# Kernel optimization log

Measured on AMD Instinct MI355X. Metric: run time of the kernel, lower is better.

## Reference

```python
import jax, jax.numpy as jnp
import numpy as np

B, S = 64, 512
DC, DB = 200, 200            # embed_char_dim, embed_bichar_dim
HID = 300                    # linear out / lstm input
H = 300                      # rnn_hidden_dim
VC, VB = 10000, 200000       # char / bichar vocab
INPUT_DIM = (DC + DB) * 2    # 800


def lstm_scan(x_seq, W_hh):
    # x_seq: [S, B, 4H] = x @ W_ih.T + b_ih + b_hh, precomputed for all steps
    Bq = x_seq.shape[1]
    h0 = jnp.zeros((Bq, H), x_seq.dtype)
    c0 = jnp.zeros((Bq, H), x_seq.dtype)

    def step(carry, x_t):
        h, c = carry
        gates = x_t + h @ W_hh.T                 # [B, 4H]
        i, f, g, o = jnp.split(gates, 4, axis=-1)
        i = jax.nn.sigmoid(i)
        f = jax.nn.sigmoid(f)
        g = jnp.tanh(g)
        o = jax.nn.sigmoid(o)
        c = f * c + i * g
        h = o * jnp.tanh(c)
        return (h, c), h

    _, hs = jax.lax.scan(step, (h0, c0), x_seq)
    return hs                                    # [S, B, H]


def setup_inputs() -> dict:
    key = jax.random.key(0)
    ks = jax.random.split(key, 20)
    inp = {
        'char_features': jax.random.randint(ks[0], (B, S), 0, VC),
        'bichar_left_features': jax.random.randint(ks[1], (B, S), 0, VB),
        'bichar_right_features': jax.random.randint(ks[2], (B, S), 0, VB),
        'static_char_features': jax.random.randint(ks[3], (B, S), 0, VC),
        'static_bichar_left_features': jax.random.randint(ks[4], (B, S), 0, VB),
        'static_bichar_right_features': jax.random.randint(ks[5], (B, S), 0, VB),
        # embedding tables (padding-id row zeroing omitted; random rows)
        'char_embed': jax.random.normal(ks[6], (VC, DC), jnp.float32) * 0.1,
        'bichar_embed': jax.random.normal(ks[7], (VB, DB), jnp.float32) * 0.1,
        'static_char_embed': jax.random.uniform(ks[8], (VC, DC), jnp.float32, -0.12, 0.12),
        'static_bichar_embed': jax.random.uniform(ks[9], (VB, DB), jnp.float32, -0.12, 0.12),
        # linear: [HID, INPUT_DIM]
        'W_lin': jax.random.normal(ks[10], (HID, INPUT_DIM), jnp.float32) * (1.0 / np.sqrt(INPUT_DIM)),
        'b_lin': jax.random.normal(ks[11], (HID,), jnp.float32) * 0.01,
        # LSTM cells (b = b_ih + b_hh folded)
        'Wih_l': jax.random.normal(ks[12], (4 * H, HID), jnp.float32) * (1.0 / np.sqrt(HID)),
        'Whh_l': jax.random.normal(ks[13], (4 * H, H), jnp.float32) * (1.0 / np.sqrt(H)),
        'b_l': jax.random.normal(ks[14], (4 * H,), jnp.float32) * 0.01,
        'Wih_r': jax.random.normal(ks[15], (4 * H, HID), jnp.float32) * (1.0 / np.sqrt(HID)),
        'Whh_r': jax.random.normal(ks[16], (4 * H, H), jnp.float32) * (1.0 / np.sqrt(H)),
        'b_r': jax.random.normal(ks[17], (4 * H,), jnp.float32) * 0.01,
    }
    return inp


def reference(char_features, bichar_left_features, bichar_right_features,
              static_char_features, static_bichar_left_features, static_bichar_right_features,
              char_embed, bichar_embed, static_char_embed, static_bichar_embed,
              W_lin, b_lin, Wih_l, Whh_l, b_l, Wih_r, Whh_r, b_r):
    # embedding lookups (dropout is identity in eval mode)
    cf = char_embed[char_features]                       # [B,S,DC]
    scf = static_char_embed[static_char_features]        # [B,S,DC]
    bl = bichar_embed[bichar_left_features]              # [B,S,DB]
    br = bichar_embed[bichar_right_features]             # [B,S,DB]
    sbl = static_bichar_embed[static_bichar_left_features]
    sbr = static_bichar_embed[static_bichar_right_features]

    left = jnp.concatenate([cf, scf, bl, sbl], axis=-1)   # [B,S,INPUT_DIM]
    right = jnp.concatenate([cf, scf, br, sbr], axis=-1)
    left = jnp.tanh(left @ W_lin.T + b_lin)               # [B,S,HID]
    right = jnp.tanh(right @ W_lin.T + b_lin)

    # precompute input contributions for all timesteps, then scan the recurrence
    xl = jnp.einsum('bsd,gd->sbg', left, Wih_l) + b_l     # [S,B,4H]
    hs_l = lstm_scan(xl, Whh_l)                            # [S,B,H]

    xr = jnp.einsum('bsd,gd->sbg', right, Wih_r) + b_r
    hs_r = lstm_scan(xr[::-1], Whh_r)[::-1]               # right-to-left LSTM

    out = jnp.concatenate([hs_l.transpose(1, 0, 2), hs_r.transpose(1, 0, 2)], axis=-1)
    return out                                             # [B,S,2H]
```

## Files before the change

### kernel.cpp

```cpp
#include <hip/hip_runtime.h>
#include <hip/hip_bf16.h>

#define S_LEN 512
#define BATCH 64
#define DC    200
#define HID   300
#define H4    1200
#define IN_DIM 800
#define G_SPLIT 10

typedef __attribute__((ext_vector_type(8))) short short8b;
typedef __attribute__((ext_vector_type(4))) float f32x4;
typedef __attribute__((ext_vector_type(4))) int   i32x4;

__device__ __forceinline__ float sigmoidf_(float x) { return 1.0f / (1.0f + __expf(-x)); }
__device__ __forceinline__ float tanhf_(float x)    { return 2.0f / (1.0f + __expf(-2.0f * x)) - 1.0f; }

__global__ void k_prep_w(const float* __restrict__ Whh_l, const float* __restrict__ Whh_r,
                         const float* __restrict__ Wih_l, const float* __restrict__ Wih_r,
                         __hip_bfloat16* __restrict__ Whh_p, __hip_bfloat16* __restrict__ Wih_p) {
    int i = blockIdx.x * 256 + threadIdx.x;
    if (i >= 2 * 1280 * 320) return;
    int slot = i % 320;
    int R = (i / 320) % 1280;
    int d = i / (320 * 1280);
    int g = R >> 7, local = R & 127;
    float vh = 0.f, vi = 0.f;
    if (local < 120) {
        int q = local / 30, jj = local % 30;
        int n = q * 300 + g * 30 + jj;
        const float* Whh = d ? Whh_r : Whh_l;
        const float* Wih = d ? Wih_r : Wih_l;
        int g2 = slot >> 5, jj2 = slot & 31;
        if (jj2 < 30) vh = Whh[n * 300 + g2 * 30 + jj2];
        if (slot < 300) vi = Wih[n * 300 + slot];
    }
    Whh_p[i] = __float2bfloat16(vh);
    Wih_p[i] = __float2bfloat16(vi);
}

__global__ void k_prep_misc(const float* __restrict__ b_l, const float* __restrict__ b_r,
                            int* __restrict__ hb_st,
                            float* __restrict__ bias_p) {
    int i = blockIdx.x * 256 + threadIdx.x;
    if (i < 102400) hb_st[i] = 0;
    if (i < 2 * 1280) {
        int d = i / 1280, R = i % 1280;
        int g = R >> 7, local = R & 127;
        float v = 0.f;
        if (local < 120) { int q = local / 30, jj = local % 30; v = (d ? b_r : b_l)[q * 300 + g * 30 + jj]; }
        bias_p[i] = v;
    }
}

__global__ __launch_bounds__(256) void k_lin(
    const int* __restrict__ cf, const int* __restrict__ bl, const int* __restrict__ br,
    const int* __restrict__ scf, const int* __restrict__ sbl, const int* __restrict__ sbr,
    const float* __restrict__ ce, const float* __restrict__ be,
    const float* __restrict__ sce, const float* __restrict__ sbe,
    const float* __restrict__ W, const float* __restrict__ bias,
    __hip_bfloat16* __restrict__ outL, __hip_bfloat16* __restrict__ outR)
{
    const int z = blockIdx.y;
    const int* dynIdx  = z ? br  : bl;
    const int* statIdx = z ? sbr : sbl;
    __hip_bfloat16* outp = z ? outR : outL;
    const int m0 = blockIdx.x * 64;

    __shared__ __align__(16) __hip_bfloat16 sA[64][40];
    __shared__ __align__(16) __hip_bfloat16 sB[320][40];
    const int t = threadIdx.x, lane = t & 63, wv = t >> 6;

    const int rA = t >> 2, c8A = (t & 3) * 8;
    const int mA = m0 + rA;
    const int idc = cf[mA], idsc = scf[mA], idd = dynIdx[mA], ids = statIdx[mA];

    f32x4 acc[4][5] = {};

    for (int k0 = 0; k0 < IN_DIM; k0 += 32) {
        {
            int k = k0 + c8A;
            int seg = k / 200, kin = k - seg * 200;
            const float* tab = (seg == 0) ? ce : (seg == 1) ? sce : (seg == 2) ? be : sbe;
            int id = (seg == 0) ? idc : (seg == 1) ? idsc : (seg == 2) ? idd : ids;
            const float* tp = tab + (size_t)id * DC + kin;
            f32x4 v0 = *reinterpret_cast<const f32x4*>(tp);
            f32x4 v1 = *reinterpret_cast<const f32x4*>(tp + 4);
            union { short8b v; __hip_bfloat16 h[8]; } u;
#pragma unroll
            for (int q = 0; q < 4; ++q) { u.h[q] = __float2bfloat16(v0[q]); u.h[4 + q] = __float2bfloat16(v1[q]); }
            *reinterpret_cast<short8b*>(&sA[rA][c8A]) = u.v;
        }
#pragma unroll
        for (int j = 0; j < 5; ++j) {
            int i = t + j * 256;
            int n = i >> 2, ch = (i & 3) * 8;
            f32x4 v0 = {0, 0, 0, 0}, v1 = {0, 0, 0, 0};
            if (n < HID) {
                const float* wp = W + (size_t)n * IN_DIM + k0 + ch;
                v0 = *reinterpret_cast<const f32x4*>(wp);
                v1 = *reinterpret_cast<const f32x4*>(wp + 4);
            }
            union { short8b v; __hip_bfloat16 h[8]; } u;
#pragma unroll
            for (int q = 0; q < 4; ++q) { u.h[q] = __float2bfloat16(v0[q]); u.h[4 + q] = __float2bfloat16(v1[q]); }
            *reinterpret_cast<short8b*>(&sB[n][ch]) = u.v;
        }
        __syncthreads();
        const int kl = (lane >> 4) * 8, bb = lane & 15;
#pragma unroll
        for (int mt = 0; mt < 4; ++mt) {
            short8b af = *reinterpret_cast<const short8b*>(&sA[mt * 16 + bb][kl]);
#pragma unroll
            for (int nt = 0; nt < 5; ++nt) {
                short8b bf = *reinterpret_cast<const short8b*>(&sB[(wv * 5 + nt) * 16 + bb][kl]);
                acc[mt][nt] = __builtin_amdgcn_mfma_f32_16x16x32_bf16(af, bf, acc[mt][nt], 0, 0, 0);
            }
        }
        __syncthreads();
    }
    const int bb = lane & 15;
#pragma unroll
    for (int mt = 0; mt < 4; ++mt)
#pragma unroll
        for (int nt = 0; nt < 5; ++nt) {
            int p = (wv * 5 + nt) * 16 + bb;
            float bv = (p < HID) ? bias[p] : 0.f;
#pragma unroll
            for (int r = 0; r < 4; ++r) {
                int m = m0 + mt * 16 + (lane >> 4) * 4 + r;
                float val = (p < HID) ? tanhf_(acc[mt][nt][r] + bv) : 0.f;
                outp[(size_t)m * 320 + p] = __float2bfloat16(val);
            }
        }
}

__global__ __launch_bounds__(256) void k_xgemm(
    const __hip_bfloat16* __restrict__ A,
    const __hip_bfloat16* __restrict__ Wih_p,
    const float* __restrict__ bias_p,
    __hip_bfloat16* __restrict__ Xout)
{
    const int dir = blockIdx.z;
    const int m0 = blockIdx.x * 64;
    const int n0 = blockIdx.y * 128;
    const __hip_bfloat16* Ad = A + (size_t)dir * 32768 * 320;
    const __hip_bfloat16* Wd = Wih_p + (size_t)dir * 1280 * 320;
    const float* bd = bias_p + dir * 1280;
    __hip_bfloat16* Xd = Xout + (size_t)dir * 512 * 64 * 1280;

    __shared__ __align__(16) __hip_bfloat16 sA[64][40];
    __shared__ __align__(16) __hip_bfloat16 sB[128][40];
    const int t = threadIdx.x, lane = t & 63, wv = t >> 6;
    f32x4 acc[4][2] = {};

    for (int k0 = 0; k0 < 320; k0 += 32) {
        {
            int r = t >> 2, kg = (t & 3) * 8;
            *reinterpret_cast<short8b*>(&sA[r][kg]) =
                *reinterpret_cast<const short8b*>(Ad + (size_t)(m0 + r) * 320 + k0 + kg);
        }
#pragma unroll
        for (int i = 0; i < 2; ++i) {
            int c = t + i * 256;
            int r = c >> 2, kg = (c & 3) * 8;
            *reinterpret_cast<short8b*>(&sB[r][kg]) =
                *reinterpret_cast<const short8b*>(Wd + (size_t)(n0 + r) * 320 + k0 + kg);
        }
        __syncthreads();
        const int kl = (lane >> 4) * 8;
#pragma unroll
        for (int mt = 0; mt < 4; ++mt) {
            short8b af = *reinterpret_cast<const short8b*>(&sA[mt * 16 + (lane & 15)][kl]);
#pragma unroll
            for (int nt = 0; nt < 2; ++nt) {
                short8b bf = *reinterpret_cast<const short8b*>(&sB[(wv * 2 + nt) * 16 + (lane & 15)][kl]);
                acc[mt][nt] = __builtin_amdgcn_mfma_f32_16x16x32_bf16(af, bf, acc[mt][nt], 0, 0, 0);
            }
        }
        __syncthreads();
    }
#pragma unroll
    for (int mt = 0; mt < 4; ++mt)
#pragma unroll
        for (int nt = 0; nt < 2; ++nt) {
            int p = n0 + (wv * 2 + nt) * 16 + (lane & 15);
            float bv = bd[p];
#pragma unroll
            for (int r = 0; r < 4; ++r) {
                int m = m0 + mt * 16 + (lane >> 4) * 4 + r;
                int b = m >> 9, s = m & 511;
                Xd[(size_t)(s * 64 + b) * 1280 + p] = __float2bfloat16(acc[mt][nt][r] + bv);
            }
        }
}

__global__ __launch_bounds__(256) void k_rec(
    const __hip_bfloat16* __restrict__ X,
    const __hip_bfloat16* __restrict__ Whh_p,
    i32x4* __restrict__ hb_st,
    float* __restrict__ out)
{
    const int bid = blockIdx.x;
    const int dir = bid / (4 * G_SPLIT);
    const int grp = (bid / G_SPLIT) % 4;
    const int g   = bid % G_SPLIT;
    const int t = threadIdx.x;
    const int lane = t & 63, wv = t >> 6;
    const int b0 = grp * 16;

    __shared__ __align__(16) __hip_bfloat16 sHi[16][328];
    __shared__ __align__(16) __hip_bfloat16 sLo[16][328];
    __shared__ float sG[16][132];
    unsigned* sHiW = (unsigned*)sHi;
    unsigned* sLoW = (unsigned*)sLo;

    const int n0 = wv * 32;
    const int bb = lane & 15;
    const int hi4 = lane >> 4;

    short8b wB0[10], wB1[10];
    {
        const __hip_bfloat16* Wsrc = Whh_p + ((size_t)dir * 1280 + g * 128) * 320;
#pragma unroll
        for (int kt = 0; kt < 10; ++kt) {
            wB0[kt] = *reinterpret_cast<const short8b*>(Wsrc + (size_t)(n0 + bb) * 320 + kt * 32 + hi4 * 8);
            wB1[kt] = *reinterpret_cast<const short8b*>(Wsrc + (size_t)(n0 + 16 + bb) * 320 + kt * 32 + hi4 * 8);
        }
    }
    for (int i = t; i < 16 * 164; i += 256) { sHiW[i] = 0; sLoW[i] = 0; }
    __syncthreads();

    float cst[6] = {};

    __hip_bfloat16 xa[8];
    {
        const int s0 = dir ? (S_LEN - 1) : 0;
        const __hip_bfloat16* xp = X + (((size_t)dir * 512 + s0) * 64 + b0) * 1280 + g * 128;
#pragma unroll
        for (int r = 0; r < 4; ++r) {
            int m = hi4 * 4 + r;
            xa[r]     = xp[(size_t)m * 1280 + n0 + bb];
            xa[4 + r] = xp[(size_t)m * 1280 + n0 + 16 + bb];
        }
    }

    for (int tau = 0; tau < S_LEN; ++tau) {
        const int s = dir ? (S_LEN - 1 - tau) : tau;
        const int par = tau & 1;

        i32x4 ch[7];
        const i32x4* hbase = hb_st + ((size_t)(dir * 2 + par) * 64 + b0) * 100;
        for (;;) {
            bool ok = true;
#pragma unroll
            for (int k = 0; k < 7; ++k) {
                int idx = t + k * 256;
                if (idx < 1600)
                    asm volatile("global_load_dwordx4 %0, %1, off sc0 sc1"
                                 : "=v"(ch[k]) : "v"(hbase + idx) : "memory");
            }
            asm volatile("s_waitcnt vmcnt(0)" ::: "memory");
#pragma unroll
            for (int k = 0; k < 7; ++k) {
                int idx = t + k * 256;
                if (idx < 1600 && ch[k][0] != tau) ok = false;
            }
            if (ok) break;
            __builtin_amdgcn_s_sleep(1);
        }
        __builtin_amdgcn_sched_barrier(0);

#pragma unroll
        for (int k = 0; k < 7; ++k) {
            int idx = t + k * 256;
            if (idx < 1600) {
                int b = idx / 100, rem = idx - b * 100;
                int g2 = rem / 10, c = rem - g2 * 10;
                int chi = (c < 5) ? c : c - 5;
                unsigned* dst = ((c < 5) ? sHiW : sLoW) + b * 164 + g2 * 16 + chi * 3;
                dst[0] = (unsigned)ch[k][1];
                dst[1] = (unsigned)ch[k][2];
                dst[2] = (unsigned)ch[k][3];
            }
        }
        __syncthreads();

        f32x4 acc0, acc1;
#pragma unroll
        for (int r = 0; r < 4; ++r) {
            acc0[r] = __bfloat162float(xa[r]);
            acc1[r] = __bfloat162float(xa[4 + r]);
        }
#pragma unroll
        for (int kt = 0; kt < 10; ++kt) {
            short8b ahi = *reinterpret_cast<const short8b*>(&sHi[bb][kt * 32 + hi4 * 8]);
            short8b alo = *reinterpret_cast<const short8b*>(&sLo[bb][kt * 32 + hi4 * 8]);
            acc0 = __builtin_amdgcn_mfma_f32_16x16x32_bf16(ahi, wB0[kt], acc0, 0, 0, 0);
            acc1 = __builtin_amdgcn_mfma_f32_16x16x32_bf16(ahi, wB1[kt], acc1, 0, 0, 0);
            acc0 = __builtin_amdgcn_mfma_f32_16x16x32_bf16(alo, wB0[kt], acc0, 0, 0, 0);
            acc1 = __builtin_amdgcn_mfma_f32_16x16x32_bf16(alo, wB1[kt], acc1, 0, 0, 0);
        }
#pragma unroll
        for (int r = 0; r < 4; ++r) {
            int m = hi4 * 4 + r;
            sG[m][n0 + bb] = acc0[r];
            sG[m][n0 + 16 + bb] = acc1[r];
        }
        __syncthreads();

        if (t < 80) {
            int b = t / 5, c5 = t - (b * 5), jj0 = c5 * 6;
            float hv[6];
            unsigned hius[6], lous[6];
#pragma unroll
            for (int u = 0; u < 6; ++u) {
                int jj = jj0 + u;
                float ig = sigmoidf_(sG[b][jj]);
                float fg = sigmoidf_(sG[b][30 + jj]);
                float gg = tanhf_(sG[b][60 + jj]);
                float og = sigmoidf_(sG[b][90 + jj]);
                float cn = fg * cst[u] + ig * gg;
                cst[u] = cn;
                float h = og * tanhf_(cn);
                hv[u] = h;
                __hip_bfloat16 hb_ = __float2bfloat16(h);
                float lof = h - __bfloat162float(hb_);
                __hip_bfloat16 lb_ = __float2bfloat16(lof);
                union { __hip_bfloat16 x; unsigned short u16; } ch1{hb_}, ch2{lb_};
                hius[u] = ch1.u16;
                lous[u] = ch2.u16;
            }
            i32x4 dhi, dlo;
            dhi[0] = tau + 1; dhi[1] = (int)(hius[0] | (hius[1] << 16));
            dhi[2] = (int)(hius[2] | (hius[3] << 16)); dhi[3] = (int)(hius[4] | (hius[5] << 16));
            dlo[0] = tau + 1; dlo[1] = (int)(lous[0] | (lous[1] << 16));
            dlo[2] = (int)(lous[2] | (lous[3] << 16)); dlo[3] = (int)(lous[4] | (lous[5] << 16));
            i32x4* pb = hb_st + ((size_t)(dir * 2 + (par ^ 1)) * 64 + b0 + b) * 100 + g * 10 + c5;
            asm volatile("s_waitcnt vmcnt(0)" ::: "memory");
            asm volatile("global_store_dwordx4 %0, %1, off sc0 sc1" :: "v"(pb), "v"(dhi) : "memory");
            asm volatile("global_store_dwordx4 %0, %1, off sc0 sc1" :: "v"(pb + 5), "v"(dlo) : "memory");
            float* op = out + ((size_t)(b0 + b) * S_LEN + s) * 600 + dir * 300 + g * 30 + jj0;
#pragma unroll
            for (int u = 0; u < 6; ++u) op[u] = hv[u];
        }

        if (tau < S_LEN - 1) {
            const int sn = dir ? (s - 1) : (s + 1);
            const __hip_bfloat16* xp = X + (((size_t)dir * 512 + sn) * 64 + b0) * 1280 + g * 128;
#pragma unroll
            for (int r = 0; r < 4; ++r) {
                int m = hi4 * 4 + r;
                xa[r]     = xp[(size_t)m * 1280 + n0 + bb];
                xa[4 + r] = xp[(size_t)m * 1280 + n0 + 16 + bb];
            }
        }
    }
}

extern "C" void kernel_launch(void* const* d_in, const int* in_sizes, int n_in,
                              void* d_out, int out_size, void* d_ws, size_t ws_size,
                              hipStream_t stream) {
    const int*   cf    = (const int*)d_in[0];
    const int*   bl    = (const int*)d_in[1];
    const int*   br    = (const int*)d_in[2];
    const int*   scf   = (const int*)d_in[3];
    const int*   sbl   = (const int*)d_in[4];
    const int*   sbr   = (const int*)d_in[5];
    const float* ce    = (const float*)d_in[6];
    const float* be    = (const float*)d_in[7];
    const float* sce   = (const float*)d_in[8];
    const float* sbe   = (const float*)d_in[9];
    const float* Wlin  = (const float*)d_in[10];
    const float* blin  = (const float*)d_in[11];
    const float* Wih_l = (const float*)d_in[12];
    const float* Whh_l = (const float*)d_in[13];
    const float* b_l   = (const float*)d_in[14];
    const float* Wih_r = (const float*)d_in[15];
    const float* Whh_r = (const float*)d_in[16];
    const float* b_r   = (const float*)d_in[17];
    float* out = (float*)d_out;

    char* ws = (char*)d_ws;
    __hip_bfloat16* A_b    = (__hip_bfloat16*)(ws);
    __hip_bfloat16* A_l    = A_b;
    __hip_bfloat16* A_r    = A_b + (size_t)32768 * 320;
    __hip_bfloat16* X      = (__hip_bfloat16*)(ws + 41943040);
    __hip_bfloat16* Whh_p  = (__hip_bfloat16*)(ws + 209715200);
    __hip_bfloat16* Wih_p  = (__hip_bfloat16*)(ws + 211353600);
    float*          bias_p = (float*)(ws + 212992000);
    i32x4*          hb_st  = (i32x4*)(ws + 213002240);

    k_prep_w<<<dim3((2 * 1280 * 320 + 255) / 256), dim3(256), 0, stream>>>(
        Whh_l, Whh_r, Wih_l, Wih_r, Whh_p, Wih_p);
    k_prep_misc<<<dim3(1280), dim3(256), 0, stream>>>(b_l, b_r, (int*)hb_st, bias_p);
    k_lin<<<dim3(512, 2), dim3(256), 0, stream>>>(cf, bl, br, scf, sbl, sbr,
                                                  ce, be, sce, sbe, Wlin, blin,
                                                  A_l, A_r);
    k_xgemm<<<dim3(512, 10, 2), dim3(256), 0, stream>>>(A_b, Wih_p, bias_p, X);
    k_rec<<<dim3(80), dim3(256), 0, stream>>>(X, Whh_p, hb_st, out);
}
```

Baseline: 2.288 ms.

## Poll only unfinished hidden-state chunks and write own slice directly to LDS

The recurrent kernel's spin-wait now remembers which 16-byte hidden-state chunks already carry the current step tag and reloads only the missing ones. Chunks produced by the same block are no longer read back from global memory; the producing threads write them straight into shared memory. The global layout interleaves the hi and lo chunks in pairs. The sleep between polls grows, which cuts coherent-load traffic during the cross-block barrier but may add wake-up latency on the critical path.

```diff
diff --git a/kernel.cpp b/kernel.cpp
--- a/kernel.cpp
+++ b/kernel.cpp
@@ -40,10 +40,10 @@
 }
 
 __global__ void k_prep_misc(const float* __restrict__ b_l, const float* __restrict__ b_r,
-                            int* __restrict__ hb_st,
+                            int* __restrict__ hb,
                             float* __restrict__ bias_p) {
     int i = blockIdx.x * 256 + threadIdx.x;
-    if (i < 102400) hb_st[i] = 0;
+    if (i < 102400) hb[i] = 0;
     if (i < 2 * 1280) {
         int d = i / 1280, R = i % 1280;
         int g = R >> 7, local = R & 127;
@@ -198,7 +198,7 @@
 __global__ __launch_bounds__(256) void k_rec(
     const __hip_bfloat16* __restrict__ X,
     const __hip_bfloat16* __restrict__ Whh_p,
-    i32x4* __restrict__ hb_st,
+    i32x4* __restrict__ hb,
     float* __restrict__ out)
 {
     const int bid = blockIdx.x;
@@ -231,6 +231,16 @@
     for (int i = t; i < 16 * 164; i += 256) { sHiW[i] = 0; sLoW[i] = 0; }
     __syncthreads();
 
+    unsigned own_mask = 0;
+#pragma unroll
+    for (int k = 0; k < 7; ++k) {
+        int idx = t + k * 256;
+        if (idx < 1600) {
+            int pair = (idx % 100) >> 1;
+            if (pair / 5 == g) own_mask |= 1u << k;
+        }
+    }
+
     float cst[6] = {};
 
     __hip_bfloat16 xa[8];
@@ -249,39 +259,43 @@
         const int s = dir ? (S_LEN - 1 - tau) : tau;
         const int par = tau & 1;
 
-        i32x4 ch[7];
-        const i32x4* hbase = hb_st + ((size_t)(dir * 2 + par) * 64 + b0) * 100;
+        i32x4 q[7];
+        unsigned done = own_mask;
+        const i32x4* hbase = hb + ((size_t)(dir * 2 + par) * 64 + b0) * 100;
         for (;;) {
-            bool ok = true;
 #pragma unroll
             for (int k = 0; k < 7; ++k) {
                 int idx = t + k * 256;
-                if (idx < 1600)
+                if (idx < 1600 && !((done >> k) & 1))
                     asm volatile("global_load_dwordx4 %0, %1, off sc0 sc1"
-                                 : "=v"(ch[k]) : "v"(hbase + idx) : "memory");
+                                 : "=v"(q[k]) : "v"(hbase + idx) : "memory");
             }
             asm volatile("s_waitcnt vmcnt(0)" ::: "memory");
+            bool all = true;
 #pragma unroll
             for (int k = 0; k < 7; ++k) {
                 int idx = t + k * 256;
-                if (idx < 1600 && ch[k][0] != tau) ok = false;
-            }
-            if (ok) break;
-            __builtin_amdgcn_s_sleep(1);
+                if (idx < 1600 && !((done >> k) & 1)) {
+                    if (q[k][0] == tau) done |= 1u << k;
+                    else all = false;
+                }
+            }
+            if (all) break;
+            __builtin_amdgcn_s_sleep(4);
         }
         __builtin_amdgcn_sched_barrier(0);
 
 #pragma unroll
         for (int k = 0; k < 7; ++k) {
             int idx = t + k * 256;
-            if (idx < 1600) {
-                int b = idx / 100, rem = idx - b * 100;
-                int g2 = rem / 10, c = rem - g2 * 10;
-                int chi = (c < 5) ? c : c - 5;
-                unsigned* dst = ((c < 5) ? sHiW : sLoW) + b * 164 + g2 * 16 + chi * 3;
-                dst[0] = (unsigned)ch[k][1];
-                dst[1] = (unsigned)ch[k][2];
-                dst[2] = (unsigned)ch[k][3];
+            if (idx < 1600 && !((own_mask >> k) & 1)) {
+                int b = idx / 100, c2 = idx - b * 100;
+                int pair = c2 >> 1, buf = c2 & 1;
+                int g2 = pair / 5, chi = pair - g2 * 5;
+                unsigned* dst = (buf ? sLoW : sHiW) + b * 164 + g2 * 16 + chi * 3;
+                dst[0] = (unsigned)q[k][1];
+                dst[1] = (unsigned)q[k][2];
+                dst[2] = (unsigned)q[k][3];
             }
         }
         __syncthreads();
@@ -310,7 +324,7 @@
         __syncthreads();
 
         if (t < 80) {
-            int b = t / 5, c5 = t - (b * 5), jj0 = c5 * 6;
+            int b = t / 5, cc = t - (b * 5), jj0 = cc * 6;
             float hv[6];
             unsigned hius[6], lous[6];
 #pragma unroll
@@ -336,10 +350,14 @@
             dhi[2] = (int)(hius[2] | (hius[3] << 16)); dhi[3] = (int)(hius[4] | (hius[5] << 16));
             dlo[0] = tau + 1; dlo[1] = (int)(lous[0] | (lous[1] << 16));
             dlo[2] = (int)(lous[2] | (lous[3] << 16)); dlo[3] = (int)(lous[4] | (lous[5] << 16));
-            i32x4* pb = hb_st + ((size_t)(dir * 2 + (par ^ 1)) * 64 + b0 + b) * 100 + g * 10 + c5;
+            i32x4* pb = hb + ((size_t)(dir * 2 + (par ^ 1)) * 64 + b0 + b) * 100 + (g * 5 + cc) * 2;
             asm volatile("s_waitcnt vmcnt(0)" ::: "memory");
             asm volatile("global_store_dwordx4 %0, %1, off sc0 sc1" :: "v"(pb), "v"(dhi) : "memory");
-            asm volatile("global_store_dwordx4 %0, %1, off sc0 sc1" :: "v"(pb + 5), "v"(dlo) : "memory");
+            asm volatile("global_store_dwordx4 %0, %1, off sc0 sc1" :: "v"(pb + 1), "v"(dlo) : "memory");
+            unsigned* dHi = sHiW + b * 164 + g * 16 + cc * 3;
+            unsigned* dLo = sLoW + b * 164 + g * 16 + cc * 3;
+            dHi[0] = (unsigned)dhi[1]; dHi[1] = (unsigned)dhi[2]; dHi[2] = (unsigned)dhi[3];
+            dLo[0] = (unsigned)dlo[1]; dLo[1] = (unsigned)dlo[2]; dLo[2] = (unsigned)dlo[3];
             float* op = out + ((size_t)(b0 + b) * S_LEN + s) * 600 + dir * 300 + g * 30 + jj0;
 #pragma unroll
             for (int u = 0; u < 6; ++u) op[u] = hv[u];
@@ -389,14 +407,14 @@
     __hip_bfloat16* Whh_p  = (__hip_bfloat16*)(ws + 209715200);
     __hip_bfloat16* Wih_p  = (__hip_bfloat16*)(ws + 211353600);
     float*          bias_p = (float*)(ws + 212992000);
-    i32x4*          hb_st  = (i32x4*)(ws + 213002240);
+    i32x4*          hb     = (i32x4*)(ws + 213002240);
 
     k_prep_w<<<dim3((2 * 1280 * 320 + 255) / 256), dim3(256), 0, stream>>>(
         Whh_l, Whh_r, Wih_l, Wih_r, Whh_p, Wih_p);
-    k_prep_misc<<<dim3(1280), dim3(256), 0, stream>>>(b_l, b_r, (int*)hb_st, bias_p);
+    k_prep_misc<<<dim3(1280), dim3(256), 0, stream>>>(b_l, b_r, (int*)hb, bias_p);
     k_lin<<<dim3(512, 2), dim3(256), 0, stream>>>(cf, bl, br, scf, sbl, sbr,
                                                   ce, be, sce, sbe, Wlin, blin,
                                                   A_l, A_r);
     k_xgemm<<<dim3(512, 10, 2), dim3(256), 0, stream>>>(A_b, Wih_p, bias_p, X);
-    k_rec<<<dim3(80), dim3(256), 0, stream>>>(X, Whh_p, hb_st, out);
-}
+    k_rec<<<dim3(80), dim3(256), 0, stream>>>(X, Whh_p, hb, out);
+}
```

Result: slower. 2.558 ms (+11.8%).
